# Kernel optimization log

Measured on AMD Instinct MI355X. Metric: run time of the kernel, lower is better.

## Reference

```python
import jax, jax.numpy as jnp
import numpy as np

K1, K2, K3 = 36, 36, 2  # rolled-patch sizes hardcoded in unfolding()


def _patch_indices(C, H, W, k1=K1, k2=K2, k3=K3):
    """Precompute gather indices replacing the triple-nested torch.roll loops.

    Column col=(k*k2+j)*k1+i of Ak_3D holds X rolled by (k,i,j) along (C,H,W):
      A[b, c*H*W+h*W+w, col] = X[b, (c-k)%C, (h-i)%H, (w-j)%W]
    The adjoint gathers with +k,+i,+j shifts.
    """
    Kc = k1 * k2 * k3
    col = np.arange(Kc)
    kk = col // (k1 * k2)
    jj = (col % (k1 * k2)) // k1
    ii = col % k1
    cg, hg, wg = np.meshgrid(np.arange(C), np.arange(H), np.arange(W), indexing='ij')
    cg = cg.reshape(-1, 1); hg = hg.reshape(-1, 1); wg = wg.reshape(-1, 1)
    fwd = ((cg - kk) % C) * (H * W) + ((hg - ii) % H) * W + ((wg - jj) % W)
    adj = ((cg + kk) % C) * (H * W) + ((hg + ii) % H) * W + ((wg + jj) % W)
    return jnp.asarray(fwd, jnp.int32), jnp.asarray(adj, jnp.int32)


def _unfold(input_img, S0, alpha, beta, gamma, iters):
    B, C, H, W = input_img.shape
    m = C * H * W
    mk = (H * W) // 64
    Kc = K1 * K2 * K3
    fwd_idx, adj_idx = _patch_indices(C, H, W)
    colr = jnp.arange(Kc, dtype=jnp.int32)

    def Ak(x):  # [B,C,H,W] -> [B, m, Kc] (single gather == Ak_3D)
        return x.reshape(B, m)[:, fwd_idx]

    def Ak_adj(A):  # [B, m, Kc] -> [B,C,H,W] (== Ak_adj_3D)
        g = A[:, adj_idx, colr[None, :]]  # [B, m, Kc]
        return (g.sum(-1) / Kc).reshape(B, C, H, W)

    a3 = alpha[:, None, None]
    g3 = gamma[:, None, None]
    g4 = gamma[:, None, None, None]
    b4 = beta[:, None, None, None]
    I_mk = jnp.eye(mk, dtype=input_img.dtype)

    # t == 0 initialization (L detached, S random-clamped from setup, M/N rect. identities)
    L0 = jax.lax.stop_gradient(input_img)
    M0 = jnp.broadcast_to(jnp.eye(m, mk, dtype=input_img.dtype), (B, m, mk))
    N0 = jnp.broadcast_to(jnp.eye(mk, Kc, dtype=input_img.dtype), (B, mk, Kc))

    def step(carry, _):
        Lc, Sc, Mc, Nc = carry
        MN = Mc @ Nc                                        # [B, m, Kc]
        Ln = jnp.clip((input_img - Sc + g4 * Ak_adj(MN)) / (g4 + 1.0), 0.0, 1.0)
        Sn = (input_img - Ln) / (b4 + 1.0)
        AkL = Ak(Ln)                                        # [B, m, Kc]
        # M-update: 2g * Ak_L N^T pinv(a I + 2g N N^T)
        Cm = a3 * I_mk + 2.0 * g3 * (Nc @ Nc.transpose(0, 2, 1))      # [B, mk, mk]
        Mn = 2.0 * g3 * ((AkL @ Nc.transpose(0, 2, 1)) @ jnp.linalg.pinv(Cm))
        # N-update: 2g * pinv(a I + 2g M^T M) M^T Ak_L
        Cn = a3 * I_mk + 2.0 * g3 * (Mn.transpose(0, 2, 1) @ Mn)      # [B, mk, mk]
        Nn = 2.0 * g3 * (jnp.linalg.pinv(Cn) @ (Mn.transpose(0, 2, 1) @ AkL))
        return (Ln, Sn, Mn, Nn), None

    (Lf, _, _, _), _ = jax.lax.scan(step, (L0, S0, M0, N0), None, length=iters - 1)
    return Lf


def setup_inputs() -> dict:
    key = jax.random.key(0)
    k1, k2 = jax.random.split(key)
    B, C, H, W = 1, 2, 64, 64
    input_img = jax.random.uniform(k1, (B, C, H, W), jnp.float32)
    S0 = jnp.clip(jax.random.normal(k2, (B, C, H, W), jnp.float32), 0.0, 1.0)  # clamp(randn_like,0,1)
    alpha = jnp.full((B,), 10.0, jnp.float32)  # w_alpha
    beta = jnp.full((B,), 2.0, jnp.float32)    # w_beta
    gamma = jnp.full((B,), 10.0, jnp.float32)  # w_gamma
    return {"input_img": input_img, "S0": S0, "alpha": alpha, "beta": beta,
            "gamma": gamma, "iters": 6}


def reference(input_img, S0, alpha, beta, gamma, iters):
    return _unfold(input_img, S0, alpha, beta, gamma, iters)
```

## Files before the change

kernel.cpp:

```cpp
#include <hip/hip_runtime.h>

#define KC 2592
#define KCP 2624
#define HW 4096

#define OFF_L    0u
#define OFF_S    8192u
#define OFF_MT   16384u
#define OFF_NTT  540672u
#define OFF_BIG  708608u
#define OFF_GRAM 2805760u
#define OFF_CMI  2809856u
#define OFF_CNI  2813952u
#define OFF_ST   2818048u

__global__ __launch_bounds__(256) void k_init(const float* __restrict__ inp, const float* __restrict__ s0,
                                              float* __restrict__ L, float* __restrict__ S,
                                              float* __restrict__ Mt, float* __restrict__ NtT){
  int t = blockIdx.x * 256 + threadIdx.x;
  if (t < 8192){ L[t] = inp[t]; S[t] = s0[t]; }
  if (t < 524288){ int r = t >> 13; int p = t & 8191; Mt[t] = (p == r) ? 1.0f : 0.0f; }
  if (t < 167936){ int r = t / KCP; int d = t - r * KCP;
                   int dr = (r % 36) * 36 + r / 36;
                   NtT[t] = (d == dr) ? 1.0f : 0.0f; }
}

__device__ __forceinline__ float readlane_f(float x, int lane){
  return __uint_as_float(__builtin_amdgcn_readlane(__float_as_uint(x), lane));
}
template<int K>
__device__ __forceinline__ void gj_step(float (&b)[64], int lane){
  float bk = b[K];
  float akk = readlane_f(bk, K);
  float p = 1.0f / akk;
  bool isk = (lane == K);
  float t = isk ? 1.0f : bk;
  float pt = p * t;
  #pragma unroll
  for (int g = 0; g < 4; g++){
    float f[16];
    #pragma unroll
    for (int u = 0; u < 16; u++){
      int i = g * 16 + u;
      if (i == K) continue;
      f[u] = readlane_f(b[i], K);
    }
    #pragma unroll
    for (int u = 0; u < 16; u++){
      int i = g * 16 + u;
      if (i == K) continue;
      float base = isk ? 0.0f : b[i];
      b[i] = fmaf(-f[u], pt, base);
    }
  }
  b[K] = t * p;
}
template<int K0, int K1> struct GJR {
  static __device__ __forceinline__ void run(float (&b)[64], int lane){
    gj_step<K0>(b, lane);
    GJR<K0 + 1, K1>::run(b, lane);
  }
};
template<int KE> struct GJR<KE, KE> {
  static __device__ __forceinline__ void run(float (&b)[64], int lane){}
};
template<int PH>
__device__ void inv64_phaseA(const float* __restrict__ src, const float* __restrict__ pg,
                             const float* __restrict__ pa, float* __restrict__ state, int lane){
  float scale = 2.0f * pg[0];
  float ad = pa[0];
  float b[64];
  #pragma unroll
  for (int i = 0; i < 64; i++)
    b[i] = scale * src[i * 64 + lane] + ((i == lane) ? ad : 0.0f);
  GJR<0, PH>::run(b, lane);
  #pragma unroll
  for (int i = 0; i < 64; i++) state[i * 64 + lane] = b[i];
}
template<int PH>
__device__ void inv64_phaseB(const float* __restrict__ state, float* __restrict__ dst, int lane){
  float b[64];
  #pragma unroll
  for (int i = 0; i < 64; i++) b[i] = state[i * 64 + lane];
  GJR<PH, 64>::run(b, lane);
  #pragma unroll
  for (int i = 0; i < 64; i++) dst[i * 64 + lane] = b[i];
}
__device__ void inv64_full(const float* __restrict__ src, const float* __restrict__ pg,
                           const float* __restrict__ pa, float* __restrict__ dst, int lane){
  float scale = 2.0f * pg[0];
  float ad = pa[0];
  float b[64];
  #pragma unroll
  for (int i = 0; i < 64; i++)
    b[i] = scale * src[i * 64 + lane] + ((i == lane) ? ad : 0.0f);
  GJR<0, 64>::run(b, lane);
  #pragma unroll
  for (int i = 0; i < 64; i++) dst[i * 64 + lane] = b[i];
}

__global__ __launch_bounds__(64) void k_conv_R(const float* __restrict__ Mtg,
                                               const float* __restrict__ NtT,
                                               float* __restrict__ Rpart,
                                               const float* __restrict__ Gr,
                                               const float* __restrict__ pg,
                                               const float* __restrict__ pa,
                                               float* __restrict__ state){
  __shared__ float img[2][16][68];
  __shared__ float4 filt4[162];
  if (blockIdx.z == 4){
    if (blockIdx.x == 0 && blockIdx.y == 0)
      inv64_phaseA<32>(Gr, pg, pa, state, threadIdx.x);
    return;
  }
  int r = blockIdx.x, oct = blockIdx.y, z = blockIdx.z, tid = threadIdx.x;
  int rowbase = oct * 8 + z * 9;
  const float4* gi4 = (const float4*)(Mtg + (size_t)r * 8192);
  for (int t = tid; t < 512; t += 64){
    int fw = t & 15, rr = t >> 4;
    int c = rr >> 4, q = rr & 15;
    int gr = (rowbase + q) & 63;
    float4 v4 = gi4[(c * 64 + gr) * 16 + fw];
    float* d = &img[c][q][fw * 4];
    d[0] = v4.x; d[1] = v4.y; d[2] = v4.z; d[3] = v4.w;
  }
  int iilo = z * 9;
  const float* gf = NtT + (size_t)r * KCP;
  for (int t = tid; t < 162; t += 64){
    int kk = t / 81; int rem4 = t - kk * 81;
    filt4[t] = *(const float4*)(gf + kk * 1296 + iilo * 36 + rem4 * 4);
  }
  __syncthreads();
  int c0 = tid >> 5, hl = (tid >> 2) & 7, w0 = (tid & 3) * 16;
  float acc[16];
  #pragma unroll
  for (int u = 0; u < 16; u++) acc[u] = 0.0f;
  #pragma unroll 1
  for (int kk = 0; kk < 2; kk++){
    int cimg = (c0 + kk) & 1;
    #pragma unroll 1
    for (int iix = 0; iix < 9; iix++){
      const float* ib = img[cimg][hl + iix];
      float v[32];
      #pragma unroll
      for (int t = 0; t < 8; t++){
        float4 t4 = *(const float4*)&ib[(w0 + 4 * t) & 63];
        v[4*t] = t4.x; v[4*t+1] = t4.y; v[4*t+2] = t4.z; v[4*t+3] = t4.w;
      }
      const float4* fb = &filt4[kk * 81 + iix * 9];
      #pragma unroll
      for (int g = 0; g < 9; g++){
        float4 ff = fb[g];
        #pragma unroll
        for (int u = 0; u < 16; u++) acc[u] = fmaf(ff.x, v[(4*g + 0 + u) & 31], acc[u]);
        #pragma unroll
        for (int u = 0; u < 16; u++) acc[u] = fmaf(ff.y, v[(4*g + 1 + u) & 31], acc[u]);
        #pragma unroll
        for (int u = 0; u < 16; u++) acc[u] = fmaf(ff.z, v[(4*g + 2 + u) & 31], acc[u]);
        #pragma unroll
        for (int u = 0; u < 16; u++) acc[u] = fmaf(ff.w, v[(4*g + 3 + u) & 31], acc[u]);
        if (g < 5){
          float4 nv = *(const float4*)&ib[(w0 + 32 + 4*g) & 63];
          int s = (4*g) & 31;
          v[s] = nv.x; v[s+1] = nv.y; v[s+2] = nv.z; v[s+3] = nv.w;
        }
      }
    }
  }
  int h = oct * 8 + hl;
  size_t ob = ((size_t)r + 64 * z) * 8192 + (size_t)(c0 * HW + h * 64 + w0);
  *(float4*)&Rpart[ob]      = make_float4(acc[0], acc[1], acc[2], acc[3]);
  *(float4*)&Rpart[ob + 4]  = make_float4(acc[4], acc[5], acc[6], acc[7]);
  *(float4*)&Rpart[ob + 8]  = make_float4(acc[8], acc[9], acc[10], acc[11]);
  *(float4*)&Rpart[ob + 12] = make_float4(acc[12], acc[13], acc[14], acc[15]);
}

__global__ __launch_bounds__(64) void k_conv_T1(const float* __restrict__ Lg,
                                                const float* __restrict__ NtT,
                                                float* __restrict__ T1t,
                                                const float* __restrict__ state,
                                                float* __restrict__ CmI){
  __shared__ float img[2][16][68];
  __shared__ float4 filt4[162];
  if (blockIdx.z == 4){
    if (blockIdx.x == 0 && blockIdx.y == 0)
      inv64_phaseB<32>(state, CmI, threadIdx.x);
    return;
  }
  int r = blockIdx.x, oct = blockIdx.y, z = blockIdx.z, tid = threadIdx.x;
  int rowbase = (oct * 8 - z * 9 - 8 + 128) & 63;
  const float4* gi4 = (const float4*)Lg;
  for (int t = tid; t < 512; t += 64){
    int fw = t & 15, rr = t >> 4;
    int c = rr >> 4, q = rr & 15;
    int gr = (rowbase + q) & 63;
    float4 v4 = gi4[(c * 64 + gr) * 16 + fw];
    float* d = &img[c][q][fw * 4];
    d[0] = v4.x; d[1] = v4.y; d[2] = v4.z; d[3] = v4.w;
  }
  int iilo = z * 9;
  const float* gf = NtT + (size_t)r * KCP;
  for (int t = tid; t < 162; t += 64){
    int kk = t / 81; int rem4 = t - kk * 81;
    filt4[t] = *(const float4*)(gf + kk * 1296 + iilo * 36 + rem4 * 4);
  }
  __syncthreads();
  int c0 = tid >> 5, hl = (tid >> 2) & 7, w0 = (tid & 3) * 16;
  float acc[16];
  #pragma unroll
  for (int u = 0; u < 16; u++) acc[u] = 0.0f;
  #pragma unroll 1
  for (int kk = 0; kk < 2; kk++){
    int cimg = (c0 - kk + 2) & 1;
    #pragma unroll 1
    for (int iix = 0; iix < 9; iix++){
      const float* ib = img[cimg][hl - iix + 8];
      float v[32];
      {
        float4 tm = *(const float4*)&ib[(w0 - 4 + 64) & 63];
        v[28] = tm.x; v[29] = tm.y; v[30] = tm.z; v[31] = tm.w;
      }
      #pragma unroll
      for (int t = 0; t < 4; t++){
        float4 t4 = *(const float4*)&ib[(w0 + 4 * t) & 63];
        v[4*t] = t4.x; v[4*t+1] = t4.y; v[4*t+2] = t4.z; v[4*t+3] = t4.w;
      }
      const float4* fb = &filt4[kk * 81 + iix * 9];
      #pragma unroll
      for (int g = 0; g < 9; g++){
        float4 ff = fb[g];
        #pragma unroll
        for (int u = 0; u < 16; u++) acc[u] = fmaf(ff.x, v[(u - (4*g + 0)) & 31], acc[u]);
        #pragma unroll
        for (int u = 0; u < 16; u++) acc[u] = fmaf(ff.y, v[(u - (4*g + 1)) & 31], acc[u]);
        #pragma unroll
        for (int u = 0; u < 16; u++) acc[u] = fmaf(ff.z, v[(u - (4*g + 2)) & 31], acc[u]);
        #pragma unroll
        for (int u = 0; u < 16; u++) acc[u] = fmaf(ff.w, v[(u - (4*g + 3)) & 31], acc[u]);
        if (g < 8){
          float4 nv = *(const float4*)&ib[(w0 - 8 - 4*g + 128) & 63];
          int s = (-8 - 4*g) & 31;
          v[s] = nv.x; v[s+1] = nv.y; v[s+2] = nv.z; v[s+3] = nv.w;
        }
      }
    }
  }
  int h = oct * 8 + hl;
  size_t ob = ((size_t)r + 64 * z) * 8192 + (size_t)(c0 * HW + h * 64 + w0);
  *(float4*)&T1t[ob]      = make_float4(acc[0], acc[1], acc[2], acc[3]);
  *(float4*)&T1t[ob + 4]  = make_float4(acc[4], acc[5], acc[6], acc[7]);
  *(float4*)&T1t[ob + 8]  = make_float4(acc[8], acc[9], acc[10], acc[11]);
  *(float4*)&T1t[ob + 12] = make_float4(acc[12], acc[13], acc[14], acc[15]);
}

__global__ __launch_bounds__(256) void k_reduce_LS(const float* __restrict__ Rpart,
                                                   const float* __restrict__ inp,
                                                   const float* __restrict__ pg, const float* __restrict__ pb,
                                                   float* __restrict__ S, float* __restrict__ Ldst){
  __shared__ float red[8][32];
  int tid = threadIdx.x;
  int pi = tid & 31, sg = tid >> 5;
  int p = blockIdx.x * 32 + pi;
  float acc = 0.0f;
  #pragma unroll 4
  for (int s = sg * 32; s < sg * 32 + 32; s++) acc += Rpart[(size_t)s * 8192 + p];
  red[sg][pi] = acc;
  __syncthreads();
  if (tid < 32){
    float a = 0.0f;
    #pragma unroll
    for (int q = 0; q < 8; q++) a += red[q][pi];
    float R = a * (1.0f / 2592.0f);
    float g = pg[0], b = pb[0];
    float Ln = (inp[p] - S[p] + g * R) / (g + 1.0f);
    Ln = fminf(fmaxf(Ln, 0.0f), 1.0f);
    S[p] = (inp[p] - Ln) / (b + 1.0f);
    Ldst[p] = Ln;
  }
}

__global__ __launch_bounds__(64) void k_gram(const float* __restrict__ rows, int stride, int len4,
                                             float* __restrict__ out, float* __restrict__ zt){
  int e = blockIdx.x; int r1 = e >> 6, r2 = e & 63;
  int lane = threadIdx.x;
  if (r2 < r1){
    int idx = (r1 * (r1 - 1)) / 2 + r2;
    int t = idx * 64 + lane;
    if (t < 41472) ((float4*)zt)[t] = make_float4(0.f, 0.f, 0.f, 0.f);
    return;
  }
  const float4* a = (const float4*)(rows + (size_t)r1 * stride);
  const float4* b = (const float4*)(rows + (size_t)r2 * stride);
  float acc = 0.0f;
  for (int p = lane; p < len4; p += 64){
    float4 x = a[p], y = b[p];
    acc = fmaf(x.x, y.x, acc); acc = fmaf(x.y, y.y, acc);
    acc = fmaf(x.z, y.z, acc); acc = fmaf(x.w, y.w, acc);
  }
  for (int off = 32; off; off >>= 1) acc += __shfl_down(acc, off, 64);
  if (lane == 0){ out[r1 * 64 + r2] = acc; out[r2 * 64 + r1] = acc; }
}

__global__ __launch_bounds__(256) void k_mn(const float* __restrict__ T1t, const float* __restrict__ CmInv,
                                            const float* __restrict__ pg, float* __restrict__ Mt){
  __shared__ float4 ci4[1024];
  int tid = threadIdx.x;
  const float4* g4 = (const float4*)CmInv;
  for (int t = tid; t < 1024; t += 256) ci4[t] = g4[t];
  __syncthreads();
  int p = blockIdx.x * 256 + tid;
  int sbase = blockIdx.y * 32;
  float g2 = 2.0f * pg[0];
  float acc[32];
  #pragma unroll
  for (int s = 0; s < 32; s++) acc[s] = 0.0f;
  for (int r = 0; r < 64; r++){
    float v = T1t[(size_t)r * 8192 + p] + T1t[(size_t)(r + 64) * 8192 + p]
            + T1t[(size_t)(r + 128) * 8192 + p] + T1t[(size_t)(r + 192) * 8192 + p];
    #pragma unroll
    for (int k = 0; k < 8; k++){
      float4 c = ci4[r * 16 + (sbase >> 2) + k];
      acc[4*k+0] = fmaf(v, c.x, acc[4*k+0]);
      acc[4*k+1] = fmaf(v, c.y, acc[4*k+1]);
      acc[4*k+2] = fmaf(v, c.z, acc[4*k+2]);
      acc[4*k+3] = fmaf(v, c.w, acc[4*k+3]);
    }
  }
  #pragma unroll
  for (int s = 0; s < 32; s++) Mt[(size_t)(sbase + s) * 8192 + p] = g2 * acc[s];
}

__global__ __launch_bounds__(256) void k_conv_T2(const float* __restrict__ Lg,
                                                 const float* __restrict__ Mtg,
                                                 float* __restrict__ T2sum,
                                                 const float* __restrict__ Gr,
                                                 const float* __restrict__ pg,
                                                 const float* __restrict__ pa,
                                                 float* __restrict__ CnI){
  __shared__ float Mi[2 * 39 * 68];
  __shared__ float4 Ls4[128];
  if (blockIdx.y == 16){
    if (blockIdx.x == 0 && threadIdx.x < 64)
      inv64_full(Gr, pg, pa, CnI, threadIdx.x);
    return;
  }
  int r = blockIdx.x, hcc = blockIdx.y, tid = threadIdx.x;
  int h0 = hcc * 4;
  const float4* gm4 = (const float4*)(Mtg + (size_t)r * 8192);
  for (int t = tid; t < 1248; t += 256){
    int fw = t & 15, rr = t >> 4;
    int c = (rr >= 39) ? 1 : 0, q = rr - c * 39;
    int gr = (h0 + q) & 63;
    float4 v4 = gm4[(c * 64 + gr) * 16 + fw];
    float* d = &Mi[(c * 39 + q) * 68 + fw * 4];
    d[0] = v4.x; d[1] = v4.y; d[2] = v4.z; d[3] = v4.w;
  }
  const float4* gl4 = (const float4*)Lg;
  if (tid < 128){
    int c = tid >> 6, rem = tid & 63;
    Ls4[tid] = gl4[c * 1024 + (h0 + (rem >> 4)) * 16 + (rem & 15)];
  }
  __syncthreads();
  if (tid >= 216) return;
  int kk = tid / 108, rest = tid % 108, ii = rest / 3, jj0 = (rest % 3) * 12;
  float acc[12];
  #pragma unroll
  for (int u = 0; u < 12; u++) acc[u] = 0.0f;
  #pragma unroll 1
  for (int c = 0; c < 2; c++){
    int cimg = (c + kk) & 1;
    #pragma unroll 1
    for (int hl = 0; hl < 4; hl++){
      const float* ib = &Mi[(cimg * 39 + hl + ii) * 68];
      const float4* lrow = &Ls4[c * 64 + hl * 16];
      float v[16];
      {
        float4 t0 = *(const float4*)&ib[jj0];
        float4 t1 = *(const float4*)&ib[jj0 + 4];
        float4 t2 = *(const float4*)&ib[jj0 + 8];
        float4 t3 = *(const float4*)&ib[jj0 + 12];
        v[0]=t0.x; v[1]=t0.y; v[2]=t0.z; v[3]=t0.w;
        v[4]=t1.x; v[5]=t1.y; v[6]=t1.z; v[7]=t1.w;
        v[8]=t2.x; v[9]=t2.y; v[10]=t2.z; v[11]=t2.w;
        v[12]=t3.x; v[13]=t3.y; v[14]=t3.z; v[15]=t3.w;
      }
      #pragma unroll
      for (int wg = 0; wg < 16; wg++){
        float4 lv = lrow[wg];
        #pragma unroll
        for (int u = 0; u < 12; u++) acc[u] = fmaf(lv.x, v[(4*wg + 0 + u) & 15], acc[u]);
        #pragma unroll
        for (int u = 0; u < 12; u++) acc[u] = fmaf(lv.y, v[(4*wg + 1 + u) & 15], acc[u]);
        #pragma unroll
        for (int u = 0; u < 12; u++) acc[u] = fmaf(lv.z, v[(4*wg + 2 + u) & 15], acc[u]);
        #pragma unroll
        for (int u = 0; u < 12; u++) acc[u] = fmaf(lv.w, v[(4*wg + 3 + u) & 15], acc[u]);
        if (wg < 15){
          float4 nv = *(const float4*)&ib[(jj0 + 4*wg + 16) & 63];
          int s = (4*wg) & 15;
          v[s] = nv.x; v[s+1] = nv.y; v[s+2] = nv.z; v[s+3] = nv.w;
        }
      }
    }
  }
  #pragma unroll
  for (int u = 0; u < 12; u++){
    int col = kk * 1296 + (jj0 + u) * 36 + ii;
    atomicAdd(&T2sum[(size_t)r * KC + col], acc[u]);
  }
}

__global__ __launch_bounds__(256) void k_nn(const float* __restrict__ T2sum, const float* __restrict__ CnInv,
                                            const float* __restrict__ pg,
                                            float* __restrict__ NtT){
  __shared__ float4 ci4[1024];
  int tid = threadIdx.x;
  const float4* g4 = (const float4*)CnInv;
  for (int t = tid; t < 1024; t += 256) ci4[t] = g4[t];
  __syncthreads();
  int col = blockIdx.x * 256 + tid;
  if (col >= KC) return;
  int rb = blockIdx.y * 16;
  float g2 = 2.0f * pg[0];
  float acc[16];
  #pragma unroll
  for (int rr = 0; rr < 16; rr++) acc[rr] = 0.0f;
  for (int s = 0; s < 64; s++){
    float tv = T2sum[(size_t)s * KC + col];
    #pragma unroll
    for (int k = 0; k < 4; k++){
      float4 c = ci4[s * 16 + (rb >> 2) + k];
      acc[4*k+0] = fmaf(tv, c.x, acc[4*k+0]);
      acc[4*k+1] = fmaf(tv, c.y, acc[4*k+1]);
      acc[4*k+2] = fmaf(tv, c.z, acc[4*k+2]);
      acc[4*k+3] = fmaf(tv, c.w, acc[4*k+3]);
    }
  }
  int kk = col / 1296, rest = col % 1296, jj = rest / 36, iv = rest % 36;
  int d = (kk * 36 + iv) * 36 + jj;
  #pragma unroll
  for (int rr = 0; rr < 16; rr++){
    NtT[(size_t)(rb + rr) * KCP + d] = g2 * acc[rr];
  }
}

extern "C" void kernel_launch(void* const* d_in, const int* in_sizes, int n_in,
                              void* d_out, int out_size, void* d_ws, size_t ws_size,
                              hipStream_t stream) {
  const float* inp = (const float*)d_in[0];
  const float* s0  = (const float*)d_in[1];
  const float* pa  = (const float*)d_in[2];
  const float* pb  = (const float*)d_in[3];
  const float* pg  = (const float*)d_in[4];
  float* ws  = (float*)d_ws;
  float* L   = ws + OFF_L;   float* S   = ws + OFF_S;    float* Mt  = ws + OFF_MT;
  float* NtT = ws + OFF_NTT; float* Big = ws + OFF_BIG;
  float* T2s = ws + OFF_BIG + 1327104u;
  float* Gr  = ws + OFF_GRAM;
  float* CmI = ws + OFF_CMI; float* CnI = ws + OFF_CNI;
  float* St  = ws + OFF_ST;
  float* out = (float*)d_out;

  k_init<<<2048, 256, 0, stream>>>(inp, s0, L, S, Mt, NtT);
  for (int step = 0; step < 5; step++){
    bool last = (step == 4);
    if (!last)
      k_gram<<<4096, 64, 0, stream>>>(NtT, KCP, KCP / 4, Gr, T2s);
    k_conv_R<<<dim3(64, 8, last ? 4 : 5), 64, 0, stream>>>(Mt, NtT, Big, Gr, pg, pa, St);
    k_reduce_LS<<<256, 256, 0, stream>>>(Big, inp, pg, pb, S, last ? out : L);
    if (last) break;
    k_conv_T1<<<dim3(64, 8, 5), 64, 0, stream>>>(L, NtT, Big, St, CmI);
    k_mn<<<dim3(32, 2), 256, 0, stream>>>(Big, CmI, pg, Mt);
    k_gram<<<4096, 64, 0, stream>>>(Mt, 8192, 2048, Gr, T2s);
    k_conv_T2<<<dim3(64, 17), 256, 0, stream>>>(L, Mt, T2s, Gr, pg, pa, CnI);
    k_nn<<<dim3(11, 4), 256, 0, stream>>>(T2s, CnI, pg, NtT);
  }
}
```

Baseline: 949.3 us.

## Recompute N-update via L autocorrelation and N filter instead of M-based conv

Rewrites the N-update by substituting Mn = AkL·N^T·CmInv. M^T·AkL then becomes a circular autocorrelation of L, convolved with the old N filters and followed by the combined CmInv·CnInv matrix Q. This replaces the M-times-L convolution that used atomics with an autocorrelation kernel, a filter convolution writing six partial buffers, and a final small matmul. The T2 zeroing in k_gram and the atomics go away, and the 64x64 inverse switches to a rolled loop. Reassociating the products changes rounding, and the rolled Gauss-Jordan loop may be slower per pivot.

New measurement: 1.143 ms. 20.4% more time.

```diff
diff --git a/kernel.cpp b/kernel.cpp
--- a/kernel.cpp
+++ b/kernel.cpp
@@ -13,6 +13,9 @@
 #define OFF_CMI  2809856u
 #define OFF_CNI  2813952u
 #define OFF_ST   2818048u
+#define OFF_UP   708608u
+#define OFF_ACLP (708608u + 1048576u)
+#define OFF_Q    (708608u + 1114112u)
 
 __global__ __launch_bounds__(256) void k_init(const float* __restrict__ inp, const float* __restrict__ s0,
                                               float* __restrict__ L, float* __restrict__ S,
@@ -86,7 +89,7 @@
   #pragma unroll
   for (int i = 0; i < 64; i++) dst[i * 64 + lane] = b[i];
 }
-__device__ void inv64_full(const float* __restrict__ src, const float* __restrict__ pg,
+__device__ void inv64_loop(const float* __restrict__ src, const float* __restrict__ pg,
                            const float* __restrict__ pa, float* __restrict__ dst, int lane){
   float scale = 2.0f * pg[0];
   float ad = pa[0];
@@ -94,7 +97,26 @@
   #pragma unroll
   for (int i = 0; i < 64; i++)
     b[i] = scale * src[i * 64 + lane] + ((i == lane) ? ad : 0.0f);
-  GJR<0, 64>::run(b, lane);
+  for (int K = 0; K < 64; K++){
+    float bK = b[0];
+    #pragma unroll
+    for (int i = 1; i < 64; i++) bK = (i == K) ? b[i] : bK;
+    float akk = readlane_f(bK, K);
+    float p = 1.0f / akk;
+    bool isk = (lane == K);
+    float t = isk ? 1.0f : bK;
+    float pt = p * t;
+    float f[64];
+    #pragma unroll
+    for (int i = 0; i < 64; i++) f[i] = readlane_f(b[i], K);
+    float rowk = t * p;
+    #pragma unroll
+    for (int i = 0; i < 64; i++){
+      float base = isk ? 0.0f : b[i];
+      float upd = fmaf(-f[i], pt, base);
+      b[i] = (i == K) ? rowk : upd;
+    }
+  }
   #pragma unroll
   for (int i = 0; i < 64; i++) dst[i * 64 + lane] = b[i];
 }
@@ -280,15 +302,10 @@
 }
 
 __global__ __launch_bounds__(64) void k_gram(const float* __restrict__ rows, int stride, int len4,
-                                             float* __restrict__ out, float* __restrict__ zt){
+                                             float* __restrict__ out){
   int e = blockIdx.x; int r1 = e >> 6, r2 = e & 63;
+  if (r2 < r1) return;
   int lane = threadIdx.x;
-  if (r2 < r1){
-    int idx = (r1 * (r1 - 1)) / 2 + r2;
-    int t = idx * 64 + lane;
-    if (t < 41472) ((float4*)zt)[t] = make_float4(0.f, 0.f, 0.f, 0.f);
-    return;
-  }
   const float4* a = (const float4*)(rows + (size_t)r1 * stride);
   const float4* b = (const float4*)(rows + (size_t)r2 * stride);
   float acc = 0.0f;
@@ -330,106 +347,185 @@
   for (int s = 0; s < 32; s++) Mt[(size_t)(sbase + s) * 8192 + p] = g2 * acc[s];
 }
 
-__global__ __launch_bounds__(256) void k_conv_T2(const float* __restrict__ Lg,
-                                                 const float* __restrict__ Mtg,
-                                                 float* __restrict__ T2sum,
-                                                 const float* __restrict__ Gr,
-                                                 const float* __restrict__ pg,
-                                                 const float* __restrict__ pa,
-                                                 float* __restrict__ CnI){
-  __shared__ float Mi[2 * 39 * 68];
-  __shared__ float4 Ls4[128];
-  if (blockIdx.y == 16){
-    if (blockIdx.x == 0 && threadIdx.x < 64)
-      inv64_full(Gr, pg, pa, CnI, threadIdx.x);
+__global__ __launch_bounds__(256) void k_acl(const float* __restrict__ Lg,
+                                             float* __restrict__ ACLp,
+                                             const float* __restrict__ Gr,
+                                             const float* __restrict__ pg,
+                                             const float* __restrict__ pa,
+                                             float* __restrict__ CnI){
+  __shared__ float Ls[128 * 68];
+  __shared__ float sred[16 * 68];
+  if (blockIdx.x == 256){
+    if (threadIdx.x < 64)
+      inv64_loop(Gr, pg, pa, CnI, threadIdx.x);
     return;
   }
-  int r = blockIdx.x, hcc = blockIdx.y, tid = threadIdx.x;
-  int h0 = hcc * 4;
-  const float4* gm4 = (const float4*)(Mtg + (size_t)r * 8192);
-  for (int t = tid; t < 1248; t += 256){
-    int fw = t & 15, rr = t >> 4;
-    int c = (rr >= 39) ? 1 : 0, q = rr - c * 39;
-    int gr = (h0 + q) & 63;
-    float4 v4 = gm4[(c * 64 + gr) * 16 + fw];
-    float* d = &Mi[(c * 39 + q) * 68 + fw * 4];
+  int bx = blockIdx.x, tid = threadIdx.x;
+  int kt = bx >> 7, it = (bx >> 1) & 63, cc = bx & 1;
+  const float4* gl4 = (const float4*)Lg;
+  for (int t = tid; t < 2048; t += 256){
+    int row = t >> 4, c4 = t & 15;
+    float4 v4 = gl4[row * 16 + c4];
+    float* d = &Ls[row * 68 + c4 * 4];
     d[0] = v4.x; d[1] = v4.y; d[2] = v4.z; d[3] = v4.w;
   }
-  const float4* gl4 = (const float4*)Lg;
-  if (tid < 128){
-    int c = tid >> 6, rem = tid & 63;
-    Ls4[tid] = gl4[c * 1024 + (h0 + (rem >> 4)) * 16 + (rem & 15)];
-  }
+  __syncthreads();
+  int j4 = tid & 15;
+  int hgw = ((tid >> 4) & 3) | ((tid >> 6) << 2);
+  float acc[4] = {0.f, 0.f, 0.f, 0.f};
+  int rb1 = cc * 64, rb2 = ((cc + kt) & 1) * 64;
+  #pragma unroll 1
+  for (int hl = 0; hl < 4; hl++){
+    int h = hl * 16 + hgw;
+    const float* r1 = &Ls[(rb1 + h) * 68];
+    const float* r2 = &Ls[(rb2 + ((h + it) & 63)) * 68];
+    float v[32];
+    #pragma unroll
+    for (int t = 0; t < 8; t++){
+      float4 t4 = *(const float4*)&r2[((j4 + t) & 15) * 4];
+      v[4*t] = t4.x; v[4*t+1] = t4.y; v[4*t+2] = t4.z; v[4*t+3] = t4.w;
+    }
+    float head[4] = {v[0], v[1], v[2], v[3]};
+    #pragma unroll
+    for (int g = 0; g < 16; g++){
+      float4 ff = *(const float4*)&r1[g * 4];
+      #pragma unroll
+      for (int e = 0; e < 4; e++){
+        float fv = (e == 0) ? ff.x : (e == 1) ? ff.y : (e == 2) ? ff.z : ff.w;
+        #pragma unroll
+        for (int u = 0; u < 4; u++){
+          int x = 4 * g + e + u;
+          float val = (x < 64) ? v[x & 31] : head[x - 64];
+          acc[u] = fmaf(fv, val, acc[u]);
+        }
+      }
+      if (g < 8){
+        float4 nv = *(const float4*)&r2[((j4 + 8 + g) & 15) * 4];
+        int s = (4 * g) & 31;
+        v[s] = nv.x; v[s+1] = nv.y; v[s+2] = nv.z; v[s+3] = nv.w;
+      }
+    }
+  }
+  #pragma unroll
+  for (int u = 0; u < 4; u++) sred[hgw * 68 + j4 * 4 + u] = acc[u];
+  __syncthreads();
+  if (tid < 64){
+    float s = 0.0f;
+    #pragma unroll
+    for (int q = 0; q < 16; q++) s += sred[q * 68 + tid];
+    ACLp[cc * 8192 + kt * 4096 + it * 64 + tid] = s;
+  }
+}
+
+__global__ __launch_bounds__(256) void k_ucv(const float* __restrict__ NtT,
+                                             const float* __restrict__ ACLp,
+                                             float* __restrict__ Up,
+                                             const float* __restrict__ CmI,
+                                             const float* __restrict__ CnI,
+                                             const float* __restrict__ pg,
+                                             float* __restrict__ Q){
+  __shared__ float Acl[128 * 68];
+  __shared__ float4 filt4[108];
+  if (blockIdx.y == 6){
+    if (blockIdx.x == 0 && threadIdx.x < 64){
+      int rr = threadIdx.x;
+      float cn[64];
+      #pragma unroll
+      for (int s = 0; s < 64; s++) cn[s] = CnI[s * 64 + rr];
+      float g2 = 2.0f * pg[0];
+      float g22 = g2 * g2;
+      for (int r = 0; r < 64; r++){
+        float q = 0.0f;
+        #pragma unroll
+        for (int s = 0; s < 64; s++) q = fmaf(CmI[r * 64 + s], cn[s], q);
+        Q[r * 64 + rr] = g22 * q;
+      }
+    }
+    return;
+  }
+  int r = blockIdx.x, y = blockIdx.y, tid = threadIdx.x;
+  const float4* ap4 = (const float4*)ACLp;
+  for (int t = tid; t < 2048; t += 256){
+    int row = t >> 4, c4 = t & 15;
+    float4 a0 = ap4[row * 16 + c4];
+    float4 a1 = ap4[2048 + row * 16 + c4];
+    float* d = &Acl[row * 68 + c4 * 4];
+    d[0] = a0.x + a1.x; d[1] = a0.y + a1.y; d[2] = a0.z + a1.z; d[3] = a0.w + a1.w;
+  }
+  const float* gf = NtT + (size_t)r * KCP + y * 432;
+  for (int t = tid; t < 108; t += 256) filt4[t] = *(const float4*)(gf + t * 4);
   __syncthreads();
   if (tid >= 216) return;
-  int kk = tid / 108, rest = tid % 108, ii = rest / 3, jj0 = (rest % 3) * 12;
+  int kk_s = y / 3;
+  int kk_d = tid / 108, rest = tid % 108, ii_d = rest / 3, jj0 = (rest % 3) * 12;
   float acc[12];
   #pragma unroll
   for (int u = 0; u < 12; u++) acc[u] = 0.0f;
   #pragma unroll 1
-  for (int c = 0; c < 2; c++){
-    int cimg = (c + kk) & 1;
-    #pragma unroll 1
-    for (int hl = 0; hl < 4; hl++){
-      const float* ib = &Mi[(cimg * 39 + hl + ii) * 68];
-      const float4* lrow = &Ls4[c * 64 + hl * 16];
-      float v[16];
-      {
-        float4 t0 = *(const float4*)&ib[jj0];
-        float4 t1 = *(const float4*)&ib[jj0 + 4];
-        float4 t2 = *(const float4*)&ib[jj0 + 8];
-        float4 t3 = *(const float4*)&ib[jj0 + 12];
-        v[0]=t0.x; v[1]=t0.y; v[2]=t0.z; v[3]=t0.w;
-        v[4]=t1.x; v[5]=t1.y; v[6]=t1.z; v[7]=t1.w;
-        v[8]=t2.x; v[9]=t2.y; v[10]=t2.z; v[11]=t2.w;
-        v[12]=t3.x; v[13]=t3.y; v[14]=t3.z; v[15]=t3.w;
-      }
-      #pragma unroll
-      for (int wg = 0; wg < 16; wg++){
-        float4 lv = lrow[wg];
-        #pragma unroll
-        for (int u = 0; u < 12; u++) acc[u] = fmaf(lv.x, v[(4*wg + 0 + u) & 15], acc[u]);
-        #pragma unroll
-        for (int u = 0; u < 12; u++) acc[u] = fmaf(lv.y, v[(4*wg + 1 + u) & 15], acc[u]);
-        #pragma unroll
-        for (int u = 0; u < 12; u++) acc[u] = fmaf(lv.z, v[(4*wg + 2 + u) & 15], acc[u]);
-        #pragma unroll
-        for (int u = 0; u < 12; u++) acc[u] = fmaf(lv.w, v[(4*wg + 3 + u) & 15], acc[u]);
-        if (wg < 15){
-          float4 nv = *(const float4*)&ib[(jj0 + 4*wg + 16) & 63];
-          int s = (4*wg) & 15;
-          v[s] = nv.x; v[s+1] = nv.y; v[s+2] = nv.z; v[s+3] = nv.w;
-        }
+  for (int l = 0; l < 12; l++){
+    int ii_s = y * 12 + l - kk_s * 36;
+    int kt = (kk_d - kk_s) & 1;
+    int it = (ii_d - ii_s) & 63;
+    const float* ib = &Acl[(kt * 64 + it) * 68];
+    float v[32];
+    {
+      float4 tm = *(const float4*)&ib[(jj0 - 4 + 64) & 63];
+      v[28] = tm.x; v[29] = tm.y; v[30] = tm.z; v[31] = tm.w;
+    }
+    #pragma unroll
+    for (int t = 0; t < 4; t++){
+      float4 t4 = *(const float4*)&ib[(jj0 + 4 * t) & 63];
+      v[4*t] = t4.x; v[4*t+1] = t4.y; v[4*t+2] = t4.z; v[4*t+3] = t4.w;
+    }
+    const float4* fb = &filt4[l * 9];
+    #pragma unroll
+    for (int g = 0; g < 9; g++){
+      float4 ff = fb[g];
+      #pragma unroll
+      for (int u = 0; u < 12; u++) acc[u] = fmaf(ff.x, v[(u - (4*g + 0)) & 31], acc[u]);
+      #pragma unroll
+      for (int u = 0; u < 12; u++) acc[u] = fmaf(ff.y, v[(u - (4*g + 1)) & 31], acc[u]);
+      #pragma unroll
+      for (int u = 0; u < 12; u++) acc[u] = fmaf(ff.z, v[(u - (4*g + 2)) & 31], acc[u]);
+      #pragma unroll
+      for (int u = 0; u < 12; u++) acc[u] = fmaf(ff.w, v[(u - (4*g + 3)) & 31], acc[u]);
+      if (g < 8){
+        float4 nv = *(const float4*)&ib[(jj0 - 8 - 4*g + 128) & 63];
+        int s = (-8 - 4*g) & 31;
+        v[s] = nv.x; v[s+1] = nv.y; v[s+2] = nv.z; v[s+3] = nv.w;
       }
     }
   }
   #pragma unroll
   for (int u = 0; u < 12; u++){
-    int col = kk * 1296 + (jj0 + u) * 36 + ii;
-    atomicAdd(&T2sum[(size_t)r * KC + col], acc[u]);
-  }
-}
-
-__global__ __launch_bounds__(256) void k_nn(const float* __restrict__ T2sum, const float* __restrict__ CnInv,
-                                            const float* __restrict__ pg,
-                                            float* __restrict__ NtT){
-  __shared__ float4 ci4[1024];
+    int col = kk_d * 1296 + (jj0 + u) * 36 + ii_d;
+    Up[(size_t)y * 165888 + (size_t)r * KC + col] = acc[u];
+  }
+}
+
+__global__ __launch_bounds__(256) void k_nn2(const float* __restrict__ Up, const float* __restrict__ Q,
+                                             float* __restrict__ NtT){
+  __shared__ float4 q4[1024];
   int tid = threadIdx.x;
-  const float4* g4 = (const float4*)CnInv;
-  for (int t = tid; t < 1024; t += 256) ci4[t] = g4[t];
+  const float4* g4 = (const float4*)Q;
+  for (int t = tid; t < 1024; t += 256) q4[t] = g4[t];
   __syncthreads();
   int col = blockIdx.x * 256 + tid;
   if (col >= KC) return;
   int rb = blockIdx.y * 16;
-  float g2 = 2.0f * pg[0];
   float acc[16];
   #pragma unroll
   for (int rr = 0; rr < 16; rr++) acc[rr] = 0.0f;
-  for (int s = 0; s < 64; s++){
-    float tv = T2sum[(size_t)s * KC + col];
+  for (int r = 0; r < 64; r++){
+    float tv = Up[(size_t)r * KC + col]
+             + Up[(size_t)165888 + (size_t)r * KC + col]
+             + Up[(size_t)331776 + (size_t)r * KC + col]
+             + Up[(size_t)497664 + (size_t)r * KC + col]
+             + Up[(size_t)663552 + (size_t)r * KC + col]
+             + Up[(size_t)829440 + (size_t)r * KC + col];
     #pragma unroll
     for (int k = 0; k < 4; k++){
-      float4 c = ci4[s * 16 + (rb >> 2) + k];
+      float4 c = q4[r * 16 + (rb >> 2) + k];
       acc[4*k+0] = fmaf(tv, c.x, acc[4*k+0]);
       acc[4*k+1] = fmaf(tv, c.y, acc[4*k+1]);
       acc[4*k+2] = fmaf(tv, c.z, acc[4*k+2]);
@@ -440,7 +536,7 @@
   int d = (kk * 36 + iv) * 36 + jj;
   #pragma unroll
   for (int rr = 0; rr < 16; rr++){
-    NtT[(size_t)(rb + rr) * KCP + d] = g2 * acc[rr];
+    NtT[(size_t)(rb + rr) * KCP + d] = acc[rr];
   }
 }
 
@@ -455,7 +551,9 @@
   float* ws  = (float*)d_ws;
   float* L   = ws + OFF_L;   float* S   = ws + OFF_S;    float* Mt  = ws + OFF_MT;
   float* NtT = ws + OFF_NTT; float* Big = ws + OFF_BIG;
-  float* T2s = ws + OFF_BIG + 1327104u;
+  float* Up   = ws + OFF_UP;
+  float* ACLp = ws + OFF_ACLP;
+  float* Q    = ws + OFF_Q;
   float* Gr  = ws + OFF_GRAM;
   float* CmI = ws + OFF_CMI; float* CnI = ws + OFF_CNI;
   float* St  = ws + OFF_ST;
@@ -465,14 +563,15 @@
   for (int step = 0; step < 5; step++){
     bool last = (step == 4);
     if (!last)
-      k_gram<<<4096, 64, 0, stream>>>(NtT, KCP, KCP / 4, Gr, T2s);
+      k_gram<<<4096, 64, 0, stream>>>(NtT, KCP, KCP / 4, Gr);
     k_conv_R<<<dim3(64, 8, last ? 4 : 5), 64, 0, stream>>>(Mt, NtT, Big, Gr, pg, pa, St);
     k_reduce_LS<<<256, 256, 0, stream>>>(Big, inp, pg, pb, S, last ? out : L);
     if (last) break;
     k_conv_T1<<<dim3(64, 8, 5), 64, 0, stream>>>(L, NtT, Big, St, CmI);
     k_mn<<<dim3(32, 2), 256, 0, stream>>>(Big, CmI, pg, Mt);
-    k_gram<<<4096, 64, 0, stream>>>(Mt, 8192, 2048, Gr, T2s);
-    k_conv_T2<<<dim3(64, 17), 256, 0, stream>>>(L, Mt, T2s, Gr, pg, pa, CnI);
-    k_nn<<<dim3(11, 4), 256, 0, stream>>>(T2s, CnI, pg, NtT);
-  }
-}
+    k_gram<<<4096, 64, 0, stream>>>(Mt, 8192, 2048, Gr);
+    k_acl<<<257, 256, 0, stream>>>(L, ACLp, Gr, pg, pa, CnI);
+    k_ucv<<<dim3(64, 7), 256, 0, stream>>>(NtT, ACLp, Up, CmI, CnI, pg, Q);
+    k_nn2<<<dim3(11, 4), 256, 0, stream>>>(Up, Q, NtT);
+  }
+}
```
